# Kernel tuning notes

Hardware: AMD Instinct MI355X
Metric: run time of the kernel (lower is better)

## Reference

```python
import jax, jax.numpy as jnp
import numpy as np

N_HEADS, D_MODEL, D_HEAD = 16, 1024, 64
EPSILON = -100000.0  # module uses -1e5, not -inf
INIT_STD = 0.02


def setup_inputs() -> dict:
    key = jax.random.key(0)
    ks = jax.random.split(key, 5)
    B, S = 4, 2048
    x = jax.random.normal(ks[0], (B, S, D_MODEL), dtype=jnp.float32)
    W_Q = INIT_STD * jax.random.normal(ks[1], (N_HEADS, D_MODEL, D_HEAD), dtype=jnp.float32)
    W_K = INIT_STD * jax.random.normal(ks[2], (N_HEADS, D_MODEL, D_HEAD), dtype=jnp.float32)
    W_V = INIT_STD * jax.random.normal(ks[3], (N_HEADS, D_MODEL, D_HEAD), dtype=jnp.float32)
    W_O = INIT_STD * jax.random.normal(ks[4], (N_HEADS, D_HEAD, D_MODEL), dtype=jnp.float32)
    b_Q = jnp.zeros((N_HEADS, D_HEAD), jnp.float32)
    b_K = jnp.zeros((N_HEADS, D_HEAD), jnp.float32)
    b_V = jnp.zeros((N_HEADS, D_HEAD), jnp.float32)
    b_O = jnp.zeros((D_MODEL,), jnp.float32)
    return {"normalized_resid_pre": x, "W_Q": W_Q, "b_Q": b_Q, "W_K": W_K,
            "b_K": b_K, "W_V": W_V, "b_V": b_V, "W_O": W_O, "b_O": b_O}


def reference(normalized_resid_pre, W_Q, b_Q, W_K, b_K, W_V, b_V, W_O, b_O):
    x = normalized_resid_pre  # [b, s, e]
    q = jnp.einsum('bse,neh->bsnh', x, W_Q) + b_Q
    k = jnp.einsum('bse,neh->bsnh', x, W_K) + b_K
    v = jnp.einsum('bse,neh->bsnh', x, W_V) + b_V
    scores = jnp.einsum('bqnh,bknh->bnqk', q, k) / jnp.sqrt(jnp.float32(D_HEAD))
    sq, sk = scores.shape[-2], scores.shape[-1]
    causal = jnp.triu(jnp.ones((sq, sk), bool), k=1)  # True above diagonal
    scores = jnp.where(causal, jnp.float32(EPSILON), scores)
    probs = jax.nn.softmax(scores, axis=-1)
    z = jnp.einsum('bnqk,bknh->bqnh', probs, v)
    # sum over heads of per-head output projection + bias
    attn_out = jnp.einsum('bqnh,nhe->bqe', z, W_O) + b_O
    return attn_out
```

## Files before the change

kernel.cpp:

```cpp
#include <hip/hip_runtime.h>


typedef __attribute__((ext_vector_type(8))) short short8;
typedef __attribute__((ext_vector_type(4))) float floatx4;

#define SCL 0.1803368801111244f

__device__ __forceinline__ unsigned short f2bf(float f) {
  unsigned int x = __float_as_uint(f);
  x += 0x7fffu + ((x >> 16) & 1u);
  return (unsigned short)(x >> 16);
}

__device__ __forceinline__ void gload_lds16(const unsigned short* g, unsigned short* lds) {
  __builtin_amdgcn_global_load_lds(
      (const __attribute__((address_space(1))) void*)g,
      (__attribute__((address_space(3))) void*)lds, 16, 0, 0);
}

__global__ __launch_bounds__(256) void prep_kernel(
    const float* __restrict__ X,  unsigned short* __restrict__ Xb,
    const float* __restrict__ Wq, const float* __restrict__ Wk,
    const float* __restrict__ Wv, unsigned short* __restrict__ Bt,
    const float* __restrict__ Wo, unsigned short* __restrict__ Wt)
{
  __shared__ unsigned short T[64 * 72];
  const int bid = blockIdx.x, t = threadIdx.x;
  if (bid < 8192) {
    int idx = ((bid << 8) + t) << 2;
    float4 f = *(const float4*)(X + idx);
    unsigned short u[4] = { f2bf(f.x), f2bf(f.y), f2bf(f.z), f2bf(f.w) };
    *(uint2*)(Xb + idx) = *(uint2*)u;
  } else if (bid < 8960) {
    int b2 = bid - 8192;
    int e0 = (b2 & 15) << 6, nn = (b2 >> 4) & 15, proj = b2 >> 8;
    const float* W = (proj == 0) ? Wq : (proj == 1) ? Wk : Wv;
    const float* src = W + ((size_t)nn << 16) + ((size_t)e0 << 6);
#pragma unroll
    for (int rnd = 0; rnd < 4; ++rnd) {
      int off = (rnd << 10) + (t << 2);
      float4 f = *(const float4*)(src + off);
      int r = off >> 6, h = off & 63;
      T[r * 72 + h]     = f2bf(f.x);
      T[r * 72 + h + 1] = f2bf(f.y);
      T[r * 72 + h + 2] = f2bf(f.z);
      T[r * 72 + h + 3] = f2bf(f.w);
    }
    __syncthreads();
    const int h = t >> 2, ck = t & 3;
    size_t orow = ((size_t)((proj << 10) + (nn << 6) + h) << 10) + e0 + (ck << 4);
#pragma unroll
    for (int g = 0; g < 2; ++g) {
      unsigned short v[8];
#pragma unroll
      for (int j = 0; j < 8; ++j) v[j] = T[((ck << 4) + (g << 3) + j) * 72 + h];
      *(int4*)(Bt + orow + (g << 3)) = *(int4*)v;
    }
  } else {
    int b2 = bid - 8960;
    int e0 = (b2 & 15) << 6, k0 = (b2 >> 4) << 6;
#pragma unroll
    for (int rnd = 0; rnd < 4; ++rnd) {
      int r = (rnd << 4) + (t >> 4);
      int c = (t & 15) << 2;
      float4 f = *(const float4*)(Wo + ((size_t)(k0 + r) << 10) + e0 + c);
      T[r * 72 + c]     = f2bf(f.x);
      T[r * 72 + c + 1] = f2bf(f.y);
      T[r * 72 + c + 2] = f2bf(f.z);
      T[r * 72 + c + 3] = f2bf(f.w);
    }
    __syncthreads();
    const int i = t >> 2, ck = t & 3;
    size_t orow = ((size_t)(e0 + i) << 10) + k0 + (ck << 4);
#pragma unroll
    for (int g = 0; g < 2; ++g) {
      unsigned short v[8];
#pragma unroll
      for (int j = 0; j < 8; ++j) v[j] = T[((ck << 4) + (g << 3) + j) * 72 + i];
      *(int4*)(Wt + orow + (g << 3)) = *(int4*)v;
    }
  }
}

template <int MODE>
__global__ __launch_bounds__(256) void gemm128_kernel(
    const unsigned short* __restrict__ A,
    const unsigned short* __restrict__ Bt,
    const float* __restrict__ b0, const float* __restrict__ b1,
    const float* __restrict__ b2,
    unsigned short* __restrict__ Oq, unsigned short* __restrict__ Ok,
    unsigned short* __restrict__ Ov, float* __restrict__ Of)
{
  const int K = 1024;
  __shared__ __align__(16) unsigned short As[8192];
  __shared__ __align__(16) unsigned short Bs[8192];
  const int tid = threadIdx.x;
  const int l   = tid & 63, w = tid >> 6;
  const int l15 = l & 15,  lg = l >> 4;
  const int mo  = (w >> 1) << 6, no = (w & 1) << 6;
  const int m0  = blockIdx.y << 7, n0 = blockIdx.x << 7;
  const int srow = l >> 3;
  const int gblk = ((l & 7) ^ srow) << 3;
  const int rsw  = l15 & 7;

  floatx4 acc[4][4];
#pragma unroll
  for (int i = 0; i < 4; ++i)
#pragma unroll
    for (int j = 0; j < 4; ++j) acc[i][j] = (floatx4){0.f, 0.f, 0.f, 0.f};

  for (int k0 = 0; k0 < K; k0 += 64) {
    __syncthreads();
#pragma unroll
    for (int s = 0; s < 4; ++s) {
      const int br = (s << 5) + (w << 3);
      gload_lds16(A  + (size_t)(m0 + br + srow) * K + k0 + gblk, &As[br << 6]);
      gload_lds16(Bt + (size_t)(n0 + br + srow) * K + k0 + gblk, &Bs[br << 6]);
    }
    __syncthreads();
#pragma unroll
    for (int kh = 0; kh < 2; ++kh) {
      const int bo = (((kh << 2) + lg) ^ rsw) << 3;
      short8 af[4], bf[4];
#pragma unroll
      for (int mc = 0; mc < 4; ++mc)
        af[mc] = *(const short8*)&As[((mo + (mc << 4) + l15) << 6) + bo];
#pragma unroll
      for (int nc = 0; nc < 4; ++nc)
        bf[nc] = *(const short8*)&Bs[((no + (nc << 4) + l15) << 6) + bo];
#pragma unroll
      for (int mc = 0; mc < 4; ++mc)
#pragma unroll
        for (int nc = 0; nc < 4; ++nc)
          acc[mc][nc] = __builtin_amdgcn_mfma_f32_16x16x32_bf16(af[mc], bf[nc], acc[mc][nc], 0, 0, 0);
    }
  }

#pragma unroll
  for (int nc = 0; nc < 4; ++nc) {
    int c = n0 + no + (nc << 4) + l15;
    if (MODE == 1) {
      float bv = b0[c];
#pragma unroll
      for (int mc = 0; mc < 4; ++mc)
#pragma unroll
        for (int r = 0; r < 4; ++r) {
          int m = m0 + mo + (mc << 4) + (lg << 2) + r;
          Of[((size_t)m << 10) + c] = acc[mc][nc][r] + bv;
        }
    } else {
      int proj = c >> 10, cc = c & 1023;
      int hn = cc >> 6, h = cc & 63;
      const float* bp = (proj == 0) ? b0 : (proj == 1) ? b1 : b2;
      float bv = bp[cc];
      float sc = (proj == 0) ? SCL : 1.0f;
      if (proj < 2) {
        unsigned short* O = (proj == 0) ? Oq : Ok;
#pragma unroll
        for (int mc = 0; mc < 4; ++mc)
#pragma unroll
          for (int r = 0; r < 4; ++r) {
            int m = m0 + mo + (mc << 4) + (lg << 2) + r;
            int bb = m >> 11, ss = m & 2047;
            O[((((size_t)(bb << 4) + hn) << 11) + ss) * 64 + h] = f2bf((acc[mc][nc][r] + bv) * sc);
          }
      } else {
#pragma unroll
        for (int mc = 0; mc < 4; ++mc) {
          int m = m0 + mo + (mc << 4) + (lg << 2);
          int bb = m >> 11, ss = m & 2047;
          unsigned short p0 = f2bf(acc[mc][nc][0] + bv);
          unsigned short p1 = f2bf(acc[mc][nc][1] + bv);
          unsigned short p2 = f2bf(acc[mc][nc][2] + bv);
          unsigned short p3 = f2bf(acc[mc][nc][3] + bv);
          uint2 pk;
          pk.x = (unsigned int)p0 | ((unsigned int)p1 << 16);
          pk.y = (unsigned int)p2 | ((unsigned int)p3 << 16);
          *(uint2*)&Ov[((((size_t)(bb << 4) + hn) << 6) + h) * 2048 + ss] = pk;
        }
      }
    }
  }
}

__global__ __launch_bounds__(256, 4) void flash9_kernel(
    const unsigned short* __restrict__ Q,
    const unsigned short* __restrict__ K,
    const unsigned short* __restrict__ Vt,
    unsigned short* __restrict__ Z)
{
  __shared__ __align__(16) unsigned short Ks[8192];
  __shared__ __align__(16) unsigned short Vs[4096];
  __shared__ __align__(16) unsigned short Ps[8192];

  const int tid = threadIdx.x;
  const int l   = tid & 63, w = tid >> 6;
  const int l15 = l & 15,  lg = l >> 4;
  const int x    = blockIdx.x;
  const int qt   = 15 - (x >> 6);
  const int head = x & 63;
  const int n = head & 15, b = head >> 4;
  const size_t hoff = (size_t)head << 17;
  const unsigned short* Qh = Q + hoff;
  const unsigned short* Kh = K + hoff;
  const unsigned short* Vh = Vt + hoff;
  unsigned short* Psw = Ps + (w << 11);

  const int srow8 = l >> 3;
  const int sblk8 = ((l & 7) ^ srow8) << 3;
  const int swz   = l15 & 7;
  const int bo0   = (lg ^ swz) << 3;
  const int bo1   = ((4 + lg) ^ swz) << 3;

  const unsigned short* gK = Kh + (size_t)(((w << 4) + srow8) << 6) + sblk8;
  const unsigned short* gV = Vh + (size_t)(((w << 4) + srow8) << 11) + sblk8;
  unsigned short* ldsK0 = &Ks[w << 10];
  unsigned short* ldsV0 = &Vs[w << 10];

  uint2* pw[2][4];
  const short8* pr[2][2];
#pragma unroll
  for (int qc = 0; qc < 2; ++qc) {
    const int rbase = ((qc << 4) + l15) << 6;
#pragma unroll
    for (int mc = 0; mc < 4; ++mc)
      pw[qc][mc] = (uint2*)&Psw[rbase + (((((mc << 1) + (lg >> 1)) ^ swz) << 3) + ((lg & 1) << 2))];
#pragma unroll
    for (int kc = 0; kc < 2; ++kc)
      pr[qc][kc] = (const short8*)&Psw[rbase + ((((kc << 2) + lg) ^ swz) << 3)];
  }

  short8 onef;
#pragma unroll
  for (int i = 0; i < 8; ++i) onef[i] = (short)0x3F80;

  floatx4 z4 = (floatx4){0.f, 0.f, 0.f, 0.f};
  asm volatile("" : "+v"(z4));

  const int q0w = (qt << 7) + (w << 5);

  short8 qf[2][2];
#pragma unroll
  for (int qc = 0; qc < 2; ++qc)
#pragma unroll
    for (int dh = 0; dh < 2; ++dh)
      qf[qc][dh] = *(const short8*)(Qh + (size_t)(q0w + (qc << 4) + l15) * 64 + (dh << 5) + (lg << 3));

  floatx4 acc_o[2][4], acc_l[2];
#pragma unroll
  for (int qc = 0; qc < 2; ++qc) {
    acc_l[qc] = (floatx4){0.f, 0.f, 0.f, 0.f};
#pragma unroll
    for (int dc = 0; dc < 4; ++dc) acc_o[qc][dc] = (floatx4){0.f, 0.f, 0.f, 0.f};
  }

  gload_lds16(gK,       ldsK0);
  gload_lds16(gK + 512, ldsK0 + 512);
  asm volatile("s_waitcnt vmcnt(0)" ::: "memory");
  __builtin_amdgcn_s_barrier();

  int buf = 0;
  const int nkt = (qt << 1) + 2;
  for (int kt = 0; kt < nkt; ++kt) {
    const int k0 = kt << 6;

    {
      const unsigned short* pV = gV + k0;
      gload_lds16(pV,          ldsV0);
      gload_lds16(pV + 16384,  ldsV0 + 512);
    }
    if (kt + 1 < nkt) {
      const unsigned short* pK = gK + ((size_t)(kt + 1) << 12);
      unsigned short* d = ldsK0 + ((buf ^ 1) << 12);
      gload_lds16(pK,       d);
      gload_lds16(pK + 512, d + 512);
    }

    const bool active = (k0 <= q0w + 31);
    if (active) {
      const int cb = buf << 12;

      floatx4 s0[4], s1[4];
      __builtin_amdgcn_s_setprio(1);
#pragma unroll
      for (int mc = 0; mc < 4; ++mc) {
        short8 ak = *(const short8*)&Ks[cb + (((mc << 4) + l15) << 6) + bo0];
        s0[mc] = __builtin_amdgcn_mfma_f32_16x16x32_bf16(ak, qf[0][0], z4, 0, 0, 0);
        s1[mc] = __builtin_amdgcn_mfma_f32_16x16x32_bf16(ak, qf[1][0], z4, 0, 0, 0);
      }
#pragma unroll
      for (int mc = 0; mc < 4; ++mc) {
        short8 ak = *(const short8*)&Ks[cb + (((mc << 4) + l15) << 6) + bo1];
        s0[mc] = __builtin_amdgcn_mfma_f32_16x16x32_bf16(ak, qf[0][1], s0[mc], 0, 0, 0);
        s1[mc] = __builtin_amdgcn_mfma_f32_16x16x32_bf16(ak, qf[1][1], s1[mc], 0, 0, 0);
      }
      __builtin_amdgcn_s_setprio(0);

      const bool needmask = (k0 + 63 > q0w);
#pragma unroll
      for (int qc = 0; qc < 2; ++qc) {
        const int qg = q0w + (qc << 4) + l15;
#pragma unroll
        for (int mc = 0; mc < 4; ++mc) {
          float p[4];
#pragma unroll
          for (int r = 0; r < 4; ++r) {
            float e = exp2f(qc ? s1[mc][r] : s0[mc][r]);
            if (needmask) {
              int key = k0 + (mc << 4) + (lg << 2) + r;
              e = (key > qg) ? 0.f : e;
            }
            p[r] = e;
          }
          uint2 pk;
          asm("v_cvt_pk_bf16_f32 %0, %1, %2" : "=v"(pk.x) : "v"(p[0]), "v"(p[1]));
          asm("v_cvt_pk_bf16_f32 %0, %1, %2" : "=v"(pk.y) : "v"(p[2]), "v"(p[3]));
          *pw[qc][mc] = pk;
        }
      }
    }

    asm volatile("s_waitcnt vmcnt(0)" ::: "memory");
    __builtin_amdgcn_s_barrier();

    if (active) {
      short8 pa[2][2];
#pragma unroll
      for (int qc = 0; qc < 2; ++qc)
#pragma unroll
        for (int kc = 0; kc < 2; ++kc)
          pa[qc][kc] = *pr[qc][kc];
      __builtin_amdgcn_s_setprio(1);
#pragma unroll
      for (int kc = 0; kc < 2; ++kc) {
        const int bo = kc ? bo1 : bo0;
#pragma unroll
        for (int dc = 0; dc < 4; ++dc) {
          short8 vb = *(const short8*)&Vs[(((dc << 4) + l15) << 6) + bo];
          acc_o[0][dc] = __builtin_amdgcn_mfma_f32_16x16x32_bf16(pa[0][kc], vb, acc_o[0][dc], 0, 0, 0);
          acc_o[1][dc] = __builtin_amdgcn_mfma_f32_16x16x32_bf16(pa[1][kc], vb, acc_o[1][dc], 0, 0, 0);
        }
        acc_l[0] = __builtin_amdgcn_mfma_f32_16x16x32_bf16(pa[0][kc], onef, acc_l[0], 0, 0, 0);
        acc_l[1] = __builtin_amdgcn_mfma_f32_16x16x32_bf16(pa[1][kc], onef, acc_l[1], 0, 0, 0);
      }
      __builtin_amdgcn_s_setprio(0);
    }

    __builtin_amdgcn_s_barrier();
    buf ^= 1;
  }

#pragma unroll
  for (int qc = 0; qc < 2; ++qc) {
    floatx4 inv;
#pragma unroll
    for (int r = 0; r < 4; ++r) inv[r] = 1.f / acc_l[qc][r];
#pragma unroll
    for (int dc = 0; dc < 4; ++dc)
#pragma unroll
      for (int r = 0; r < 4; ++r) {
        int qg = q0w + (qc << 4) + (lg << 2) + r;
        Z[(((size_t)b << 11) + qg) * 1024 + (n << 6) + (dc << 4) + l15] =
            f2bf(acc_o[qc][dc][r] * inv[r]);
      }
  }
}

extern "C" void kernel_launch(void* const* d_in, const int* in_sizes, int n_in,
                              void* d_out, int out_size, void* d_ws, size_t ws_size,
                              hipStream_t stream) {
  const float* x   = (const float*)d_in[0];
  const float* W_Q = (const float*)d_in[1];
  const float* b_Q = (const float*)d_in[2];
  const float* W_K = (const float*)d_in[3];
  const float* b_K = (const float*)d_in[4];
  const float* W_V = (const float*)d_in[5];
  const float* b_V = (const float*)d_in[6];
  const float* W_O = (const float*)d_in[7];
  const float* b_O = (const float*)d_in[8];
  float* out = (float*)d_out;

  unsigned short* ws    = (unsigned short*)d_ws;
  unsigned short* BtQKV = ws;
  unsigned short* Wo_t  = BtQKV + (3u << 20);
  unsigned short* Xb    = Wo_t + (1u << 20);
  unsigned short* Qb    = Xb + (8u << 20);
  unsigned short* Kb    = Qb + (8u << 20);
  unsigned short* Vtb   = Kb + (8u << 20);
  unsigned short* Zb    = Vtb + (8u << 20);

  prep_kernel<<<9216, 256, 0, stream>>>(x, Xb, W_Q, W_K, W_V, BtQKV, W_O, Wo_t);

  gemm128_kernel<0><<<dim3(24, 64), 256, 0, stream>>>(
      Xb, BtQKV, b_Q, b_K, b_V, Qb, Kb, Vtb, nullptr);

  flash9_kernel<<<1024, 256, 0, stream>>>(Qb, Kb, Vtb, Zb);

  gemm128_kernel<1><<<dim3(8, 64), 256, 0, stream>>>(
      Zb, Wo_t, b_O, nullptr, nullptr, nullptr, nullptr, nullptr, out);
}
```

Before: 263.4 us.

## Pair causal query tiles per block and double-buffer V with one barrier

The flash attention kernel now processes two query tiles per block (tile 15-p followed by tile p), so every block does the same total causal work and the grid is halved. V is now double-buffered alongside K, which removes the mid-iteration wait and barrier; the next K/V tile, including the first tile of the second half, is prefetched during compute. The costs are more LDS per block, a lower occupancy hint (3 instead of 4 blocks per CU) and fewer blocks in flight.

```diff
diff --git a/kernel.cpp b/kernel.cpp
--- a/kernel.cpp
+++ b/kernel.cpp
@@ -183,21 +183,21 @@
   }
 }
 
-__global__ __launch_bounds__(256, 4) void flash9_kernel(
+__global__ __launch_bounds__(256, 3) void flash10_kernel(
     const unsigned short* __restrict__ Q,
     const unsigned short* __restrict__ K,
     const unsigned short* __restrict__ Vt,
     unsigned short* __restrict__ Z)
 {
   __shared__ __align__(16) unsigned short Ks[8192];
-  __shared__ __align__(16) unsigned short Vs[4096];
+  __shared__ __align__(16) unsigned short Vs[8192];
   __shared__ __align__(16) unsigned short Ps[8192];
 
   const int tid = threadIdx.x;
   const int l   = tid & 63, w = tid >> 6;
   const int l15 = l & 15,  lg = l >> 4;
   const int x    = blockIdx.x;
-  const int qt   = 15 - (x >> 6);
+  const int pidx = x >> 6;
   const int head = x & 63;
   const int n = head & 15, b = head >> 4;
   const size_t hoff = (size_t)head << 17;
@@ -237,132 +237,132 @@
   floatx4 z4 = (floatx4){0.f, 0.f, 0.f, 0.f};
   asm volatile("" : "+v"(z4));
 
-  const int q0w = (qt << 7) + (w << 5);
-
-  short8 qf[2][2];
-#pragma unroll
-  for (int qc = 0; qc < 2; ++qc)
-#pragma unroll
-    for (int dh = 0; dh < 2; ++dh)
-      qf[qc][dh] = *(const short8*)(Qh + (size_t)(q0w + (qc << 4) + l15) * 64 + (dh << 5) + (lg << 3));
-
-  floatx4 acc_o[2][4], acc_l[2];
-#pragma unroll
-  for (int qc = 0; qc < 2; ++qc) {
-    acc_l[qc] = (floatx4){0.f, 0.f, 0.f, 0.f};
-#pragma unroll
-    for (int dc = 0; dc < 4; ++dc) acc_o[qc][dc] = (floatx4){0.f, 0.f, 0.f, 0.f};
-  }
-
-  gload_lds16(gK,       ldsK0);
-  gload_lds16(gK + 512, ldsK0 + 512);
+  gload_lds16(gK,         ldsK0);
+  gload_lds16(gK + 512,   ldsK0 + 512);
+  gload_lds16(gV,         ldsV0);
+  gload_lds16(gV + 16384, ldsV0 + 512);
   asm volatile("s_waitcnt vmcnt(0)" ::: "memory");
   __builtin_amdgcn_s_barrier();
 
   int buf = 0;
-  const int nkt = (qt << 1) + 2;
-  for (int kt = 0; kt < nkt; ++kt) {
-    const int k0 = kt << 6;
-
-    {
-      const unsigned short* pV = gV + k0;
-      gload_lds16(pV,          ldsV0);
-      gload_lds16(pV + 16384,  ldsV0 + 512);
-    }
-    if (kt + 1 < nkt) {
-      const unsigned short* pK = gK + ((size_t)(kt + 1) << 12);
-      unsigned short* d = ldsK0 + ((buf ^ 1) << 12);
-      gload_lds16(pK,       d);
-      gload_lds16(pK + 512, d + 512);
-    }
-
-    const bool active = (k0 <= q0w + 31);
-    if (active) {
-      const int cb = buf << 12;
-
-      floatx4 s0[4], s1[4];
-      __builtin_amdgcn_s_setprio(1);
-#pragma unroll
-      for (int mc = 0; mc < 4; ++mc) {
-        short8 ak = *(const short8*)&Ks[cb + (((mc << 4) + l15) << 6) + bo0];
-        s0[mc] = __builtin_amdgcn_mfma_f32_16x16x32_bf16(ak, qf[0][0], z4, 0, 0, 0);
-        s1[mc] = __builtin_amdgcn_mfma_f32_16x16x32_bf16(ak, qf[1][0], z4, 0, 0, 0);
+  for (int half = 0; half < 2; ++half) {
+    const int qt  = half ? pidx : (15 - pidx);
+    const int q0w = (qt << 7) + (w << 5);
+
+    short8 qf[2][2];
+#pragma unroll
+    for (int qc = 0; qc < 2; ++qc)
+#pragma unroll
+      for (int dh = 0; dh < 2; ++dh)
+        qf[qc][dh] = *(const short8*)(Qh + (size_t)(q0w + (qc << 4) + l15) * 64 + (dh << 5) + (lg << 3));
+
+    floatx4 acc_o[2][4], acc_l[2];
+#pragma unroll
+    for (int qc = 0; qc < 2; ++qc) {
+      acc_l[qc] = (floatx4){0.f, 0.f, 0.f, 0.f};
+#pragma unroll
+      for (int dc = 0; dc < 4; ++dc) acc_o[qc][dc] = (floatx4){0.f, 0.f, 0.f, 0.f};
+    }
+
+    const int nkt = (qt << 1) + 2;
+    for (int kt = 0; kt < nkt; ++kt) {
+      const int k0 = kt << 6;
+
+      const int nk0 = (kt + 1 < nkt) ? ((kt + 1) << 6) : (half == 0 ? 0 : -1);
+      if (nk0 >= 0) {
+        const int nb = (buf ^ 1) << 12;
+        const unsigned short* pK = gK + ((size_t)nk0 << 6);
+        gload_lds16(pK,       ldsK0 + nb);
+        gload_lds16(pK + 512, ldsK0 + nb + 512);
+        const unsigned short* pV = gV + nk0;
+        gload_lds16(pV,         ldsV0 + nb);
+        gload_lds16(pV + 16384, ldsV0 + nb + 512);
       }
-#pragma unroll
-      for (int mc = 0; mc < 4; ++mc) {
-        short8 ak = *(const short8*)&Ks[cb + (((mc << 4) + l15) << 6) + bo1];
-        s0[mc] = __builtin_amdgcn_mfma_f32_16x16x32_bf16(ak, qf[0][1], s0[mc], 0, 0, 0);
-        s1[mc] = __builtin_amdgcn_mfma_f32_16x16x32_bf16(ak, qf[1][1], s1[mc], 0, 0, 0);
+
+      const bool active = (k0 <= q0w + 31);
+      if (active) {
+        const int cb = buf << 12;
+
+        floatx4 s0[4], s1[4];
+        __builtin_amdgcn_s_setprio(1);
+#pragma unroll
+        for (int mc = 0; mc < 4; ++mc) {
+          short8 ak = *(const short8*)&Ks[cb + (((mc << 4) + l15) << 6) + bo0];
+          s0[mc] = __builtin_amdgcn_mfma_f32_16x16x32_bf16(ak, qf[0][0], z4, 0, 0, 0);
+          s1[mc] = __builtin_amdgcn_mfma_f32_16x16x32_bf16(ak, qf[1][0], z4, 0, 0, 0);
+        }
+#pragma unroll
+        for (int mc = 0; mc < 4; ++mc) {
+          short8 ak = *(const short8*)&Ks[cb + (((mc << 4) + l15) << 6) + bo1];
+          s0[mc] = __builtin_amdgcn_mfma_f32_16x16x32_bf16(ak, qf[0][1], s0[mc], 0, 0, 0);
+          s1[mc] = __builtin_amdgcn_mfma_f32_16x16x32_bf16(ak, qf[1][1], s1[mc], 0, 0, 0);
+        }
+        __builtin_amdgcn_s_setprio(0);
+
+        const bool needmask = (k0 + 63 > q0w);
+#pragma unroll
+        for (int qc = 0; qc < 2; ++qc) {
+          const int qg = q0w + (qc << 4) + l15;
+#pragma unroll
+          for (int mc = 0; mc < 4; ++mc) {
+            float p[4];
+#pragma unroll
+            for (int r = 0; r < 4; ++r) {
+              float e = exp2f(qc ? s1[mc][r] : s0[mc][r]);
+              if (needmask) {
+                int key = k0 + (mc << 4) + (lg << 2) + r;
+                e = (key > qg) ? 0.f : e;
+              }
+              p[r] = e;
+            }
+            uint2 pk;
+            asm("v_cvt_pk_bf16_f32 %0, %1, %2" : "=v"(pk.x) : "v"(p[0]), "v"(p[1]));
+            asm("v_cvt_pk_bf16_f32 %0, %1, %2" : "=v"(pk.y) : "v"(p[2]), "v"(p[3]));
+            *pw[qc][mc] = pk;
+          }
+        }
+
+        short8 pa[2][2];
+#pragma unroll
+        for (int qc = 0; qc < 2; ++qc)
+#pragma unroll
+          for (int kc = 0; kc < 2; ++kc)
+            pa[qc][kc] = *pr[qc][kc];
+        __builtin_amdgcn_s_setprio(1);
+#pragma unroll
+        for (int kc = 0; kc < 2; ++kc) {
+          const int bo = kc ? bo1 : bo0;
+#pragma unroll
+          for (int dc = 0; dc < 4; ++dc) {
+            short8 vb = *(const short8*)&Vs[cb + (((dc << 4) + l15) << 6) + bo];
+            acc_o[0][dc] = __builtin_amdgcn_mfma_f32_16x16x32_bf16(pa[0][kc], vb, acc_o[0][dc], 0, 0, 0);
+            acc_o[1][dc] = __builtin_amdgcn_mfma_f32_16x16x32_bf16(pa[1][kc], vb, acc_o[1][dc], 0, 0, 0);
+          }
+          acc_l[0] = __builtin_amdgcn_mfma_f32_16x16x32_bf16(pa[0][kc], onef, acc_l[0], 0, 0, 0);
+          acc_l[1] = __builtin_amdgcn_mfma_f32_16x16x32_bf16(pa[1][kc], onef, acc_l[1], 0, 0, 0);
+        }
+        __builtin_amdgcn_s_setprio(0);
       }
-      __builtin_amdgcn_s_setprio(0);
-
-      const bool needmask = (k0 + 63 > q0w);
-#pragma unroll
-      for (int qc = 0; qc < 2; ++qc) {
-        const int qg = q0w + (qc << 4) + l15;
-#pragma unroll
-        for (int mc = 0; mc < 4; ++mc) {
-          float p[4];
-#pragma unroll
-          for (int r = 0; r < 4; ++r) {
-            float e = exp2f(qc ? s1[mc][r] : s0[mc][r]);
-            if (needmask) {
-              int key = k0 + (mc << 4) + (lg << 2) + r;
-              e = (key > qg) ? 0.f : e;
-            }
-            p[r] = e;
-          }
-          uint2 pk;
-          asm("v_cvt_pk_bf16_f32 %0, %1, %2" : "=v"(pk.x) : "v"(p[0]), "v"(p[1]));
-          asm("v_cvt_pk_bf16_f32 %0, %1, %2" : "=v"(pk.y) : "v"(p[2]), "v"(p[3]));
-          *pw[qc][mc] = pk;
-        }
-      }
-    }
-
-    asm volatile("s_waitcnt vmcnt(0)" ::: "memory");
-    __builtin_amdgcn_s_barrier();
-
-    if (active) {
-      short8 pa[2][2];
-#pragma unroll
-      for (int qc = 0; qc < 2; ++qc)
-#pragma unroll
-        for (int kc = 0; kc < 2; ++kc)
-          pa[qc][kc] = *pr[qc][kc];
-      __builtin_amdgcn_s_setprio(1);
-#pragma unroll
-      for (int kc = 0; kc < 2; ++kc) {
-        const int bo = kc ? bo1 : bo0;
-#pragma unroll
-        for (int dc = 0; dc < 4; ++dc) {
-          short8 vb = *(const short8*)&Vs[(((dc << 4) + l15) << 6) + bo];
-          acc_o[0][dc] = __builtin_amdgcn_mfma_f32_16x16x32_bf16(pa[0][kc], vb, acc_o[0][dc], 0, 0, 0);
-          acc_o[1][dc] = __builtin_amdgcn_mfma_f32_16x16x32_bf16(pa[1][kc], vb, acc_o[1][dc], 0, 0, 0);
-        }
-        acc_l[0] = __builtin_amdgcn_mfma_f32_16x16x32_bf16(pa[0][kc], onef, acc_l[0], 0, 0, 0);
-        acc_l[1] = __builtin_amdgcn_mfma_f32_16x16x32_bf16(pa[1][kc], onef, acc_l[1], 0, 0, 0);
-      }
-      __builtin_amdgcn_s_setprio(0);
-    }
-
-    __builtin_amdgcn_s_barrier();
-    buf ^= 1;
-  }
-
-#pragma unroll
-  for (int qc = 0; qc < 2; ++qc) {
-    floatx4 inv;
-#pragma unroll
-    for (int r = 0; r < 4; ++r) inv[r] = 1.f / acc_l[qc][r];
-#pragma unroll
-    for (int dc = 0; dc < 4; ++dc)
-#pragma unroll
-      for (int r = 0; r < 4; ++r) {
-        int qg = q0w + (qc << 4) + (lg << 2) + r;
-        Z[(((size_t)b << 11) + qg) * 1024 + (n << 6) + (dc << 4) + l15] =
-            f2bf(acc_o[qc][dc][r] * inv[r]);
-      }
+
+      asm volatile("s_waitcnt vmcnt(0)" ::: "memory");
+      __builtin_amdgcn_s_barrier();
+      buf ^= 1;
+    }
+
+#pragma unroll
+    for (int qc = 0; qc < 2; ++qc) {
+      floatx4 inv;
+#pragma unroll
+      for (int r = 0; r < 4; ++r) inv[r] = 1.f / acc_l[qc][r];
+#pragma unroll
+      for (int dc = 0; dc < 4; ++dc)
+#pragma unroll
+        for (int r = 0; r < 4; ++r) {
+          int qg = q0w + (qc << 4) + (lg << 2) + r;
+          Z[(((size_t)b << 11) + qg) * 1024 + (n << 6) + (dc << 4) + l15] =
+              f2bf(acc_o[qc][dc][r] * inv[r]);
+        }
+    }
   }
 }
 
@@ -394,7 +394,7 @@
   gemm128_kernel<0><<<dim3(24, 64), 256, 0, stream>>>(
       Xb, BtQKV, b_Q, b_K, b_V, Qb, Kb, Vtb, nullptr);
 
-  flash9_kernel<<<1024, 256, 0, stream>>>(Qb, Kb, Vtb, Zb);
+  flash10_kernel<<<512, 256, 0, stream>>>(Qb, Kb, Vtb, Zb);
 
   gemm128_kernel<1><<<dim3(8, 64), 256, 0, stream>>>(
       Zb, Wo_t, b_O, nullptr, nullptr, nullptr, nullptr, nullptr, out);
```

New measurement: 271.1 us. 2.9% more time.
